# Kernel optimization log

Measured on AMD Instinct MI355X. Metric: run time of the kernel, lower is better.

Reference implementation:

```python
import jax, jax.numpy as jnp
import numpy as np

H, D = 8, 32          # num_heads, head dim (hidden = 256)
HID = H * D
LRELU = 0.2
NT, NC, E, FIN = 60000, 30000, 200000, 64


def setup_inputs() -> dict:
    key = jax.random.key(0)
    ks = jax.random.split(key, 24)
    s = 0.05
    inp = {
        'x_trans': jax.random.normal(ks[0], (NT, FIN), jnp.float32),
        'x_cc':    jax.random.normal(ks[1], (NC, FIN), jnp.float32),
        'src_c2t': jax.random.randint(ks[2], (E,), 0, NC),
        'dst_c2t': jax.random.randint(ks[3], (E,), 0, NT),
        'src_t2c': jax.random.randint(ks[4], (E,), 0, NT),
        'dst_t2c': jax.random.randint(ks[5], (E,), 0, NC),
        'W_in': jax.random.normal(ks[6], (2, FIN, HID), jnp.float32) * s,
        'b_in': jnp.zeros((2, HID), jnp.float32),
        'Wk': jax.random.normal(ks[7], (2, 2, HID, HID), jnp.float32) * s,
        'bk': jnp.zeros((2, 2, HID), jnp.float32),
        'Wq': jax.random.normal(ks[8], (2, 2, HID, HID), jnp.float32) * s,
        'bq': jnp.zeros((2, 2, HID), jnp.float32),
        'Wv': jax.random.normal(ks[9], (2, 2, HID, HID), jnp.float32) * s,
        'bv': jnp.zeros((2, 2, HID), jnp.float32),
        'Wa': jax.random.normal(ks[10], (2, 2, HID, HID), jnp.float32) * s,
        'ba': jnp.zeros((2, 2, HID), jnp.float32),
        'a_rel': jax.random.normal(ks[11], (2, 2, H, D, D), jnp.float32) * s,
        'm_rel': jax.random.normal(ks[12], (2, 2, H, D, D), jnp.float32) * s,
        'p_rel': jnp.ones((2, 2, H), jnp.float32),
        'skip':  jnp.ones((2, 2), jnp.float32),
        'W_out': jax.random.normal(ks[13], (HID, 64), jnp.float32) * s,
        'b_out': jnp.zeros((64,), jnp.float32),
    }
    return inp


def _hgt_layer(xs, Wk, bk, Wq, bq, Wv, bv, Wa, ba, a_rel, m_rel, p_rel, skip, edges):
    # xs: list of [N_t, HID] per node type; edges: list of (src_type, dst_type, src_idx, dst_idx)
    nt = len(xs)
    k = [(xs[t] @ Wk[t] + bk[t]).reshape(-1, H, D) for t in range(nt)]
    q = [(xs[t] @ Wq[t] + bq[t]).reshape(-1, H, D) for t in range(nt)]
    v = [(xs[t] @ Wv[t] + bv[t]).reshape(-1, H, D) for t in range(nt)]
    agg = [jnp.zeros((xs[t].shape[0], H, D), xs[t].dtype) for t in range(nt)]
    inv_sqrt_d = 1.0 / jnp.sqrt(jnp.float32(D))
    for r, (st, dt, si, di) in enumerate(edges):
        kr = jnp.einsum('nhd,hde->nhe', k[st], a_rel[r])   # relation-transformed keys
        vr = jnp.einsum('nhd,hde->nhe', v[st], m_rel[r])   # relation-transformed messages
        ke, ve, qe = kr[si], vr[si], q[dt][di]             # [E, H, D] gathers
        alpha = jnp.einsum('ehd,ehd->eh', qe, ke) * p_rel[r] * inv_sqrt_d  # [E, H]
        n_dst = xs[dt].shape[0]
        m = jax.ops.segment_max(alpha, di, num_segments=n_dst)
        ex = jnp.exp(alpha - m[di])
        ssum = jax.ops.segment_sum(ex, di, num_segments=n_dst)
        w = ex / (ssum[di] + 1e-16)                         # segment softmax per dst node
        agg[dt] = agg[dt] + jax.ops.segment_sum(ve * w[..., None], di, num_segments=n_dst)
    out = []
    for t in range(nt):
        o = jax.nn.gelu(agg[t].reshape(-1, HID), approximate=False)
        o = o @ Wa[t] + ba[t]
        beta = jax.nn.sigmoid(skip[t])
        out.append(beta * o + (1.0 - beta) * xs[t])
    return out


def reference(x_trans, x_cc, src_c2t, dst_c2t, src_t2c, dst_t2c,
              W_in, b_in, Wk, bk, Wq, bq, Wv, bv, Wa, ba,
              a_rel, m_rel, p_rel, skip, W_out, b_out):
    # per-node-type Linear + in-place relu
    xs = [jax.nn.relu(x_trans @ W_in[0] + b_in[0]),
          jax.nn.relu(x_cc @ W_in[1] + b_in[1])]
    # relation 0: cc_node -> trans_node ; relation 1: trans_node -> cc_node
    edges = [(1, 0, src_c2t, dst_c2t), (0, 1, src_t2c, dst_t2c)]
    n_layers = Wk.shape[0]
    for l in range(n_layers):
        xs = _hgt_layer(xs, Wk[l], bk[l], Wq[l], bq[l], Wv[l], bv[l], Wa[l], ba[l],
                        a_rel[l], m_rel[l], p_rel[l], skip[l], edges)
    # dropout is identity in eval mode
    y = xs[0] @ W_out + b_out
    y = jnp.where(y > 0, y, LRELU * y)                      # LeakyReLU(0.2)
    n = jnp.linalg.norm(y, axis=1, keepdims=True)
    return y / jnp.maximum(n, 1e-12)                        # F.normalize(p=2, dim=1)
```

## Files before the change

kernel.cpp:

```cpp
#include <hip/hip_runtime.h>
#include <hip/hip_bf16.h>
#include <math.h>

#define NTN 60000
#define NCN 30000
#define NED 200000

typedef unsigned short u16;
typedef unsigned long long u64;
typedef __attribute__((ext_vector_type(8))) u16 u16x8;
typedef __attribute__((ext_vector_type(8))) __bf16 bf16x8;
typedef __attribute__((ext_vector_type(4))) float f32x4;

static __device__ __forceinline__ float bf2f(u16 u) {
    return __uint_as_float(((unsigned)u) << 16);
}
static __device__ __forceinline__ u16 f2bf(float f) {
    unsigned u = __float_as_uint(f);
    unsigned r = (u + 0x7fffu + ((u >> 16) & 1u)) >> 16;
    return (u16)r;
}

__global__ void fill_u32(unsigned* __restrict__ p, unsigned v, int n) {
    int i = blockIdx.x * blockDim.x + threadIdx.x;
    int stride = gridDim.x * blockDim.x;
    for (; i < n; i += stride) p[i] = v;
}

__global__ void f32_to_bf16(const float* __restrict__ in, u16* __restrict__ out, int n4) {
    int i = blockIdx.x * blockDim.x + threadIdx.x;
    int stride = gridDim.x * blockDim.x;
    for (; i < n4; i += stride) {
        float4 v = ((const float4*)in)[i];
        ushort4 o;
        o.x = f2bf(v.x); o.y = f2bf(v.y); o.z = f2bf(v.z); o.w = f2bf(v.w);
        ((ushort4*)out)[i] = o;
    }
}

__global__ void convTb(const float* __restrict__ in, u16* __restrict__ out,
                       int K, int N, int inStride, int outStride, int nm) {
    int idx = blockIdx.x * blockDim.x + threadIdx.x;
    int per = N * (K >> 2);
    int total = per * nm;
    if (idx >= total) return;
    int mat = idx / per, rem = idx - mat * per;
    int k4 = rem / N, n = rem - k4 * N;
    int k = k4 * 4;
    const float* src = in + (size_t)mat * inStride;
    u16* dst = out + (size_t)mat * outStride;
    ushort4 o;
    o.x = f2bf(src[(size_t)(k + 0) * N + n]);
    o.y = f2bf(src[(size_t)(k + 1) * N + n]);
    o.z = f2bf(src[(size_t)(k + 2) * N + n]);
    o.w = f2bf(src[(size_t)(k + 3) * N + n]);
    *(ushort4*)(dst + (size_t)n * K + k) = o;
}

__global__ void copy_bq(const float* __restrict__ bq, float* __restrict__ bqkv) {
    int lt = blockIdx.x;
    bqkv[lt * 768 + threadIdx.x] = bq[lt * 256 + threadIdx.x];
}

__global__ __launch_bounds__(256) void fuse_weights(
    const float* __restrict__ Wk, const float* __restrict__ bk,
    const float* __restrict__ Wv, const float* __restrict__ bv,
    const float* __restrict__ a_rel, const float* __restrict__ m_rel,
    const float* __restrict__ p_rel,
    float* __restrict__ Wf2, float* __restrict__ bqkv)
{
    __shared__ float kw[256], vw[256];
    const int c = blockIdx.x, lt = blockIdx.y, tid = threadIdx.x;
    const int l = lt >> 1, t = lt & 1;
    const int lr = l * 2 + (t == 1 ? 0 : 1);
    const float* WkP = Wk + (size_t)lt * 65536;
    const float* WvP = Wv + (size_t)lt * 65536;
    const float* ar = a_rel + (size_t)lr * 8192;
    const float* mr = m_rel + (size_t)lr * 8192;
    kw[tid] = WkP[c * 256 + tid];
    vw[tid] = WvP[c * 256 + tid];
    __syncthreads();
    const int h = tid >> 5, e = tid & 31;
    const float s = p_rel[lr * 8 + h] * 0.17677669529663687f;
    float ak = 0.f, av = 0.f;
#pragma unroll 8
    for (int d = 0; d < 32; ++d) {
        ak += kw[h * 32 + d] * ar[h * 1024 + d * 32 + e];
        av += vw[h * 32 + d] * mr[h * 1024 + d * 32 + e];
    }
    float* WkfP = Wf2 + (size_t)lt * 131072;
    WkfP[c * 256 + tid] = ak * s;
    WkfP[65536 + c * 256 + tid] = av;
    if (c == 0) {
        const float* bkP = bk + (size_t)lt * 256;
        const float* bvP = bv + (size_t)lt * 256;
        float bka = 0.f, bva = 0.f;
#pragma unroll 8
        for (int d = 0; d < 32; ++d) {
            bka += bkP[h * 32 + d] * ar[h * 1024 + d * 32 + e];
            bva += bvP[h * 32 + d] * mr[h * 1024 + d * 32 + e];
        }
        bqkv[lt * 768 + 256 + tid] = bka * s;
        bqkv[lt * 768 + 512 + tid] = bva;
    }
}

template <int EPI, int BN, bool OBF>
__global__ __launch_bounds__(256) void gemm_mfma2(
    int nblk0,
    const u16* __restrict__ A0, const u16* __restrict__ W0, const float* __restrict__ b0,
    void* __restrict__ C0, int M0, int ldC0, int NY0,
    const u16* __restrict__ xr0, const float* __restrict__ sk0,
    const u16* __restrict__ A1, const u16* __restrict__ W1, const float* __restrict__ b1,
    void* __restrict__ C1, int M1, int ldC1, int NY1,
    const u16* __restrict__ xr1, const float* __restrict__ sk1,
    int K)
{
    constexpr int ASZ = 64 * 64;
    constexpr int BSZ = BN * 64;
    constexpr int NF = BN / 32;
    __shared__ u16 smem[2 * (ASZ + BSZ)];
    u16* As0 = smem;             u16* Bs0 = smem + ASZ;
    u16* As1 = smem + ASZ + BSZ; u16* Bs1 = As1 + ASZ;

    const int nwg = gridDim.x;
    const int bid = blockIdx.x;
    const int q8 = nwg >> 3, r8 = nwg & 7;
    const int xcd = bid & 7, pos = bid >> 3;
    const int lbid = (xcd < r8) ? xcd * (q8 + 1) + pos
                                : r8 * (q8 + 1) + (xcd - r8) * q8 + pos;

    const u16* A; const u16* WT; const float* bias; void* Cv;
    int M, ldC, NY, sb; const u16* xres; const float* skipPtr;
    if (lbid < nblk0) {
        A = A0; WT = W0; bias = b0; Cv = C0; M = M0; ldC = ldC0; NY = NY0;
        xres = xr0; skipPtr = sk0; sb = lbid;
    } else {
        A = A1; WT = W1; bias = b1; Cv = C1; M = M1; ldC = ldC1; NY = NY1;
        xres = xr1; skipPtr = sk1; sb = lbid - nblk0;
    }
    const int bx = sb / NY, by = sb - bx * NY;
    const int m0 = bx * 64, n0 = by * BN;

    const int tid = threadIdx.x;
    const int wave = tid >> 6, lane = tid & 63;
    const int wm = (wave >> 1) * 32, wn = (wave & 1) * (BN / 2);
    f32x4 acc[2][NF];
#pragma unroll
    for (int i = 0; i < 2; ++i)
#pragma unroll
        for (int j = 0; j < NF; ++j) acc[i][j] = (f32x4){0.f, 0.f, 0.f, 0.f};

    const int sr = lane >> 3;
    const int sl = lane & 7;

    auto stage = [&](int k0, u16* Ad, u16* Bd) {
#pragma unroll
        for (int i = 0; i < 2; ++i) {
            int rb = wave * 16 + i * 8;
            int r = rb + sr;
            int gr = m0 + r; gr = gr < M ? gr : M - 1;
            const u16* gp = A + (size_t)gr * K + k0 + ((sl ^ sr) << 3);
            __builtin_amdgcn_global_load_lds(
                (const __attribute__((address_space(1))) void*)gp,
                (__attribute__((address_space(3))) void*)(Ad + rb * 64), 16, 0, 0);
        }
#pragma unroll
        for (int i = 0; i < NF; ++i) {
            int rb = wave * (BN / 4) + i * 8;
            int r = rb + sr;
            const u16* gp = WT + (size_t)(n0 + r) * K + k0 + ((sl ^ sr) << 3);
            __builtin_amdgcn_global_load_lds(
                (const __attribute__((address_space(1))) void*)gp,
                (__attribute__((address_space(3))) void*)(Bd + rb * 64), 16, 0, 0);
        }
    };

    auto compute = [&](const u16* Ab, const u16* Bb) {
#pragma unroll
        for (int kx = 0; kx < 2; ++kx) {
            bf16x8 af[2], bfr[NF];
#pragma unroll
            for (int mf = 0; mf < 2; ++mf) {
                int r = wm + mf * 16 + (lane & 15);
                int slot = (lane >> 4) + kx * 4;
                af[mf] = __builtin_bit_cast(bf16x8,
                    *(const u16x8*)(Ab + r * 64 + ((slot ^ (r & 7)) << 3)));
            }
#pragma unroll
            for (int nf = 0; nf < NF; ++nf) {
                int r = wn + nf * 16 + (lane & 15);
                int slot = (lane >> 4) + kx * 4;
                bfr[nf] = __builtin_bit_cast(bf16x8,
                    *(const u16x8*)(Bb + r * 64 + ((slot ^ (r & 7)) << 3)));
            }
#pragma unroll
            for (int mf = 0; mf < 2; ++mf)
#pragma unroll
                for (int nf = 0; nf < NF; ++nf)
                    acc[mf][nf] = __builtin_amdgcn_mfma_f32_16x16x32_bf16(
                        af[mf], bfr[nf], acc[mf][nf], 0, 0, 0);
        }
    };

    const int nt = K >> 6;
    stage(0, As0, Bs0);
    for (int t = 0; t < nt; ++t) {
        const bool pb = t & 1;
        if (t + 1 < nt) {
            stage((t + 1) << 6, pb ? As0 : As1, pb ? Bs0 : Bs1);
            __builtin_amdgcn_sched_barrier(0);
            if constexpr (BN == 128) asm volatile("s_waitcnt vmcnt(6)" ::: "memory");
            else                     asm volatile("s_waitcnt vmcnt(4)" ::: "memory");
        } else {
            asm volatile("s_waitcnt vmcnt(0)" ::: "memory");
        }
        __builtin_amdgcn_s_barrier();
        __builtin_amdgcn_sched_barrier(0);
        compute(pb ? As1 : As0, pb ? Bs1 : Bs0);
        __builtin_amdgcn_sched_barrier(0);
        __builtin_amdgcn_s_barrier();
        __builtin_amdgcn_sched_barrier(0);
    }

    float beta = 0.f;
    if (EPI == 2) beta = 1.f / (1.f + expf(-skipPtr[0]));

    if constexpr (OBF) {
        constexpr int CLD = BN + 8;
        u16* Ct = smem;
#pragma unroll
        for (int nf = 0; nf < NF; ++nf) {
            int col = wn + nf * 16 + (lane & 15);
            int gcol = n0 + col;
            float bs = bias[gcol];
#pragma unroll
            for (int mf = 0; mf < 2; ++mf) {
#pragma unroll
                for (int j = 0; j < 4; ++j) {
                    int row = wm + mf * 16 + (lane >> 4) * 4 + j;
                    int grow = m0 + row;
                    int gr2 = grow < M ? grow : 0;
                    float c = acc[mf][nf][j] + bs;
                    if (EPI == 1) c = fmaxf(c, 0.f);
                    if (EPI == 2) c = beta * c + (1.f - beta) * bf2f(xres[(size_t)gr2 * ldC + gcol]);
                    if (EPI == 3) c = (c > 0.f) ? c : 0.2f * c;
                    Ct[row * CLD + col] = f2bf(c);
                }
            }
        }
        __syncthreads();
        int row = tid >> 2, c0 = (tid & 3) * (BN / 4);
        int grow = m0 + row;
        if (grow < M) {
            u16* dst = (u16*)Cv + (size_t)grow * ldC + n0 + c0;
            const u16* src = Ct + row * CLD + c0;
#pragma unroll
            for (int i = 0; i < BN / 32; ++i)
                *(u16x8*)(dst + i * 8) = *(const u16x8*)(src + i * 8);
        }
    } else {
#pragma unroll
        for (int nf = 0; nf < NF; ++nf) {
            int gcol = n0 + wn + nf * 16 + (lane & 15);
            float bs = bias[gcol];
#pragma unroll
            for (int mf = 0; mf < 2; ++mf) {
#pragma unroll
                for (int j = 0; j < 4; ++j) {
                    int grow = m0 + wm + mf * 16 + (lane >> 4) * 4 + j;
                    if (grow >= M) continue;
                    float c = acc[mf][nf][j] + bs;
                    if (EPI == 1) c = fmaxf(c, 0.f);
                    if (EPI == 3) c = (c > 0.f) ? c : 0.2f * c;
                    ((float*)Cv)[(size_t)grow * ldC + gcol] = c;
                }
            }
        }
    }
}

__global__ void hist_kernel(const int* __restrict__ di, unsigned* __restrict__ counts, int E) {
    int e = blockIdx.x * blockDim.x + threadIdx.x;
    if (e < E) atomicAdd(&counts[di[e]], 1u);
}

__global__ __launch_bounds__(256) void scan_blocks(
    const unsigned* __restrict__ counts, unsigned* __restrict__ pref,
    unsigned* __restrict__ bsum, int N)
{
    __shared__ unsigned tmp[256];
    int i = blockIdx.x * 256 + threadIdx.x;
    unsigned v = (i < N) ? counts[i] : 0u;
    tmp[threadIdx.x] = v;
    __syncthreads();
    for (int off = 1; off < 256; off <<= 1) {
        unsigned t = (threadIdx.x >= off) ? tmp[threadIdx.x - off] : 0u;
        __syncthreads();
        tmp[threadIdx.x] += t;
        __syncthreads();
    }
    if (i < N) pref[i] = tmp[threadIdx.x] - v;
    if (threadIdx.x == 255) bsum[blockIdx.x] = tmp[255];
}

__global__ __launch_bounds__(256) void scan_top(unsigned* __restrict__ bsum, int NB) {
    __shared__ unsigned tmp[256];
    unsigned v = (threadIdx.x < NB) ? bsum[threadIdx.x] : 0u;
    tmp[threadIdx.x] = v;
    __syncthreads();
    for (int off = 1; off < 256; off <<= 1) {
        unsigned t = (threadIdx.x >= off) ? tmp[threadIdx.x - off] : 0u;
        __syncthreads();
        tmp[threadIdx.x] += t;
        __syncthreads();
    }
    if (threadIdx.x < NB) bsum[threadIdx.x] = tmp[threadIdx.x] - v;
}

__global__ void scan_add(unsigned* __restrict__ pref, const unsigned* __restrict__ bsum,
                         const unsigned* __restrict__ counts,
                         unsigned* __restrict__ cursor, u64* __restrict__ rowinfo, int N) {
    int i = blockIdx.x * 256 + threadIdx.x;
    if (i < N) {
        unsigned s = pref[i] + bsum[blockIdx.x];
        cursor[i] = s;
        rowinfo[i] = (u64)s | ((u64)counts[i] << 32);
    }
}

__global__ void place_kernel(const int* __restrict__ di, const int* __restrict__ si,
                             unsigned* __restrict__ cursor, unsigned* __restrict__ srcout, int E) {
    int e = blockIdx.x * blockDim.x + threadIdx.x;
    if (e < E) {
        unsigned p = atomicAdd(&cursor[di[e]], 1u);
        srcout[p] = (unsigned)si[e] * 768u;
    }
}

#define TBLK ((NTN + 3) / 4)
__global__ __launch_bounds__(256) void edge_gather2(
    const u16* __restrict__ qkvT, const u16* __restrict__ qkvC,
    const u64* __restrict__ riT, const unsigned* __restrict__ srcT,
    const u64* __restrict__ riC, const unsigned* __restrict__ srcC,
    u16* __restrict__ aggT, u16* __restrict__ aggC)
{
    const int b = blockIdx.x;
    const bool isT = b < TBLK;
    const int n = (isT ? b : b - TBLK) * 4 + (threadIdx.x >> 6);
    const int Ndst = isT ? NTN : NCN;
    if (n >= Ndst) return;
    const u16* qkv_d = isT ? qkvT : qkvC;
    const u16* qkv_s = isT ? qkvC : qkvT;
    const u64* ri = isT ? riT : riC;
    const unsigned* srcarr = isT ? srcT : srcC;
    u16* agg = isT ? aggT : aggC;

    const int lane = threadIdx.x & 63;
    const int lq = lane & 31;
    const int h = lane >> 5;
    const u64 rinfo = ri[n];
    const unsigned start = (unsigned)rinfo;
    const unsigned deg = (unsigned)(rinfo >> 32);

    if (deg == 0) {
        if (lane < 32)
            *(u16x8*)&agg[(size_t)n * 256 + lq * 8] = (u16x8){0, 0, 0, 0, 0, 0, 0, 0};
        return;
    }

    u16x8 qv = *(const u16x8*)&qkv_d[(size_t)n * 768 + lq * 8];
    float qf[8];
#pragma unroll
    for (int i = 0; i < 8; ++i) qf[i] = bf2f(qv[i]);

    const u16* kvb = qkv_s + 256 + lq * 8;
    float m = -INFINITY, s = 0.f;
    float acc[8] = {0.f, 0.f, 0.f, 0.f, 0.f, 0.f, 0.f, 0.f};

    unsigned j = (unsigned)h;
    if (j < deg) {
        unsigned off = srcarr[start + j];
        u16x8 kr = *(const u16x8*)(kvb + off);
        u16x8 vr = *(const u16x8*)(kvb + off + 256);
        for (;;) {
            u16x8 kr_n, vr_n;
            const bool more = (j + 2 < deg);
            if (more) {
                unsigned off2 = srcarr[start + j + 2];
                kr_n = *(const u16x8*)(kvb + off2);
                vr_n = *(const u16x8*)(kvb + off2 + 256);
            }
            float kf[8];
#pragma unroll
            for (int i = 0; i < 8; ++i) kf[i] = bf2f(kr[i]);
            float p = qf[0] * kf[0] + qf[1] * kf[1] + qf[2] * kf[2] + qf[3] * kf[3]
                    + qf[4] * kf[4] + qf[5] * kf[5] + qf[6] * kf[6] + qf[7] * kf[7];
            p += __shfl_xor(p, 1);
            p += __shfl_xor(p, 2);
            float vf[8];
#pragma unroll
            for (int i = 0; i < 8; ++i) vf[i] = bf2f(vr[i]);
            if (__ballot(p > m) == 0ull) {
                float wv = __expf(p - m);
                s += wv;
#pragma unroll
                for (int i = 0; i < 8; ++i) acc[i] += wv * vf[i];
            } else {
                float mn = fmaxf(m, p);
                float sc = __expf(m - mn);
                float wv = __expf(p - mn);
                s = s * sc + wv;
#pragma unroll
                for (int i = 0; i < 8; ++i) acc[i] = acc[i] * sc + wv * vf[i];
                m = mn;
            }
            if (!more) break;
            kr = kr_n; vr = vr_n; j += 2;
        }
    }

    float mo = __shfl_xor(m, 32);
    float so = __shfl_xor(s, 32);
    float mt = fmaxf(m, mo);
    float sc0 = __expf(m - mt);
    float sco = __expf(mo - mt);
    float st = s * sc0 + so * sco;
    float inv = 1.f / (st + 1e-16f);
    u16x8 ov;
#pragma unroll
    for (int i = 0; i < 8; ++i) {
        float ao = __shfl_xor(acc[i], 32);
        float x = (acc[i] * sc0 + ao * sco) * inv;
        float g = 0.5f * x * (1.f + erff(x * 0.70710678118654752f));
        ov[i] = f2bf(g);
    }
    if (lane < 32)
        *(u16x8*)&agg[(size_t)n * 256 + lq * 8] = ov;
}

__global__ __launch_bounds__(256) void norm_rows(float* __restrict__ y, int M) {
    int row = blockIdx.x * 4 + (threadIdx.x >> 6);
    int lane = threadIdx.x & 63;
    if (row >= M) return;
    float v = y[(size_t)row * 64 + lane];
    float s = v * v;
#pragma unroll
    for (int off = 1; off < 64; off <<= 1) s += __shfl_xor(s, off);
    float n = sqrtf(s);
    y[(size_t)row * 64 + lane] = v / fmaxf(n, 1e-12f);
}

extern "C" void kernel_launch(void* const* d_in, const int* in_sizes, int n_in,
                              void* d_out, int out_size, void* d_ws, size_t ws_size,
                              hipStream_t stream)
{
    const float* x_trans = (const float*)d_in[0];
    const float* x_cc    = (const float*)d_in[1];
    const int* src_c2t   = (const int*)d_in[2];
    const int* dst_c2t   = (const int*)d_in[3];
    const int* src_t2c   = (const int*)d_in[4];
    const int* dst_t2c   = (const int*)d_in[5];
    const float* W_in = (const float*)d_in[6];
    const float* b_in = (const float*)d_in[7];
    const float* Wk   = (const float*)d_in[8];
    const float* bk   = (const float*)d_in[9];
    const float* Wq   = (const float*)d_in[10];
    const float* bq   = (const float*)d_in[11];
    const float* Wv   = (const float*)d_in[12];
    const float* bv   = (const float*)d_in[13];
    const float* Wa   = (const float*)d_in[14];
    const float* ba   = (const float*)d_in[15];
    const float* a_rel = (const float*)d_in[16];
    const float* m_rel = (const float*)d_in[17];
    const float* p_rel = (const float*)d_in[18];
    const float* skip  = (const float*)d_in[19];
    const float* W_out = (const float*)d_in[20];
    const float* b_out = (const float*)d_in[21];

    char* w = (char*)d_ws;
    auto alloc = [&](size_t bytes) { char* p = w; w += (bytes + 255) & ~(size_t)255; return p; };
    u16* xs0  = (u16*)alloc((size_t)NTN * 256 * 2);
    u16* xs1  = (u16*)alloc((size_t)NCN * 256 * 2);
    u16* xin0 = (u16*)alloc((size_t)NTN * 64 * 2);
    u16* xin1 = (u16*)alloc((size_t)NCN * 64 * 2);
    u16* qkv0 = (u16*)alloc((size_t)NTN * 768 * 2);
    u16* qkv1 = (u16*)alloc((size_t)NCN * 768 * 2);
    u16* agg0 = (u16*)alloc((size_t)NTN * 256 * 2);
    u16* agg1 = (u16*)alloc((size_t)NCN * 256 * 2);
    u16* WinT = (u16*)alloc((size_t)2 * 16384 * 2);
    u16* WqkvT= (u16*)alloc((size_t)4 * 196608 * 2);
    u16* WaT  = (u16*)alloc((size_t)4 * 65536 * 2);
    u16* WoutT= (u16*)alloc((size_t)16384 * 2);
    float* Wf2 = (float*)alloc((size_t)4 * 131072 * 4);
    float* bqkv = (float*)alloc((size_t)4 * 768 * 4);
    unsigned* countsT   = (unsigned*)alloc((size_t)NTN * 4);
    unsigned* prefT     = (unsigned*)alloc((size_t)NTN * 4);
    unsigned* cursorT   = (unsigned*)alloc((size_t)NTN * 4);
    u64* rowinfoT       = (u64*)alloc((size_t)NTN * 8);
    unsigned* srcAT     = (unsigned*)alloc((size_t)NED * 4);
    unsigned* countsC   = (unsigned*)alloc((size_t)NCN * 4);
    unsigned* prefC     = (unsigned*)alloc((size_t)NCN * 4);
    unsigned* cursorC   = (unsigned*)alloc((size_t)NCN * 4);
    u64* rowinfoC       = (u64*)alloc((size_t)NCN * 8);
    unsigned* srcAC     = (unsigned*)alloc((size_t)NED * 4);
    unsigned* bsum      = (unsigned*)alloc((size_t)256 * 4);
    (void)ws_size; (void)in_sizes; (void)n_in; (void)out_size;

    {
        const int EB = (NED + 255) / 256;
        int NBt = (NTN + 255) / 256;
        fill_u32<<<256, 256, 0, stream>>>(countsT, 0u, NTN);
        hist_kernel<<<EB, 256, 0, stream>>>(dst_c2t, countsT, NED);
        scan_blocks<<<NBt, 256, 0, stream>>>(countsT, prefT, bsum, NTN);
        scan_top<<<1, 256, 0, stream>>>(bsum, NBt);
        scan_add<<<NBt, 256, 0, stream>>>(prefT, bsum, countsT, cursorT, rowinfoT, NTN);
        place_kernel<<<EB, 256, 0, stream>>>(dst_c2t, src_c2t, cursorT, srcAT, NED);
        int NBc = (NCN + 255) / 256;
        fill_u32<<<256, 256, 0, stream>>>(countsC, 0u, NCN);
        hist_kernel<<<EB, 256, 0, stream>>>(dst_t2c, countsC, NED);
        scan_blocks<<<NBc, 256, 0, stream>>>(countsC, prefC, bsum, NCN);
        scan_top<<<1, 256, 0, stream>>>(bsum, NBc);
        scan_add<<<NBc, 256, 0, stream>>>(prefC, bsum, countsC, cursorC, rowinfoC, NCN);
        place_kernel<<<EB, 256, 0, stream>>>(dst_t2c, src_t2c, cursorC, srcAC, NED);
    }

    fuse_weights<<<dim3(256, 4), 256, 0, stream>>>(Wk, bk, Wv, bv, a_rel, m_rel, p_rel, Wf2, bqkv);
    copy_bq<<<4, 256, 0, stream>>>(bq, bqkv);
    convTb<<<(4 * 16384 + 255) / 256, 256, 0, stream>>>(Wq, WqkvT, 256, 256, 65536, 196608, 4);
    convTb<<<(4 * 16384 + 255) / 256, 256, 0, stream>>>(Wf2, WqkvT + 65536, 256, 256, 131072, 196608, 4);
    convTb<<<(4 * 16384 + 255) / 256, 256, 0, stream>>>(Wf2 + 65536, WqkvT + 131072, 256, 256, 131072, 196608, 4);
    convTb<<<(4 * 16384 + 255) / 256, 256, 0, stream>>>(Wa, WaT, 256, 256, 65536, 65536, 4);
    convTb<<<(2 * 4096 + 255) / 256, 256, 0, stream>>>(W_in, WinT, 64, 256, 16384, 16384, 2);
    convTb<<<(4096 + 255) / 256, 256, 0, stream>>>(W_out, WoutT, 256, 64, 16384, 16384, 1);
    f32_to_bf16<<<1024, 256, 0, stream>>>(x_trans, xin0, NTN * 64 / 4);
    f32_to_bf16<<<1024, 256, 0, stream>>>(x_cc,    xin1, NCN * 64 / 4);

    const int GT = (NTN + 63) / 64, GC = (NCN + 63) / 64;

    gemm_mfma2<1, 64, true><<<GT * 4 + GC * 4, 256, 0, stream>>>(
        GT * 4,
        xin0, WinT, b_in, xs0, NTN, 256, 4, nullptr, nullptr,
        xin1, WinT + 16384, b_in + 256, xs1, NCN, 256, 4, nullptr, nullptr,
        64);

    for (int l = 0; l < 2; ++l) {
        size_t lt0 = (size_t)(l * 2 + 0), lt1 = (size_t)(l * 2 + 1);

        gemm_mfma2<0, 64, true><<<GT * 12 + GC * 12, 256, 0, stream>>>(
            GT * 12,
            xs0, WqkvT + lt0 * 196608, bqkv + lt0 * 768, qkv0, NTN, 768, 12, nullptr, nullptr,
            xs1, WqkvT + lt1 * 196608, bqkv + lt1 * 768, qkv1, NCN, 768, 12, nullptr, nullptr,
            256);

        edge_gather2<<<TBLK + (NCN + 3) / 4, 256, 0, stream>>>(
            qkv0, qkv1,
            rowinfoT, srcAT,
            rowinfoC, srcAC,
            agg0, agg1);

        gemm_mfma2<2, 64, true><<<GT * 4 + GC * 4, 256, 0, stream>>>(
            GT * 4,
            agg0, WaT + lt0 * 65536, ba + lt0 * 256, xs0, NTN, 256, 4, xs0, skip + l * 2 + 0,
            agg1, WaT + lt1 * 65536, ba + lt1 * 256, xs1, NCN, 256, 4, xs1, skip + l * 2 + 1,
            256);
    }

    {
        float* y = (float*)d_out;
        gemm_mfma2<3, 64, false><<<GT, 256, 0, stream>>>(
            GT,
            xs0, WoutT, b_out, y, NTN, 64, 1, nullptr, nullptr,
            xs0, WoutT, b_out, y, NTN, 64, 1, nullptr, nullptr,
            256);
        norm_rows<<<NTN / 4, 256, 0, stream>>>(y, NTN);
    }
}
```

Before: 481.7 us.

## Assign one half-wave per destination node, replace erf GELU with tanh form, fuse CSR-build kernels

The edge gather now maps each 32-lane half-wave to its own destination node, so there is no cross-half softmax merge and each wave handles two nodes instead of splitting one node's edges. The exact erf GELU is replaced by a tanh-approximation evaluated with exp. The paired CSR-construction kernels (fill, histogram, scans, placement) for both relations are merged into single launches to cut launch count. Per-node parallelism over edges is halved, which lengthens the serial chain for high-degree nodes, and the tanh GELU changes numerics slightly.

```diff
diff --git a/kernel.cpp b/kernel.cpp
--- a/kernel.cpp
+++ b/kernel.cpp
@@ -21,10 +21,11 @@
     return (u16)r;
 }
 
-__global__ void fill_u32(unsigned* __restrict__ p, unsigned v, int n) {
+__global__ void fill2(unsigned* __restrict__ a, int na, unsigned* __restrict__ b, int nb) {
     int i = blockIdx.x * blockDim.x + threadIdx.x;
-    int stride = gridDim.x * blockDim.x;
-    for (; i < n; i += stride) p[i] = v;
+    int st = gridDim.x * blockDim.x;
+    for (int k = i; k < na; k += st) a[k] = 0u;
+    for (int k = i; k < nb; k += st) b[k] = 0u;
 }
 
 __global__ void f32_to_bf16(const float* __restrict__ in, u16* __restrict__ out, int n4) {
@@ -280,15 +281,24 @@
     }
 }
 
-__global__ void hist_kernel(const int* __restrict__ di, unsigned* __restrict__ counts, int E) {
+__global__ void hist2(const int* __restrict__ d0, unsigned* __restrict__ c0,
+                      const int* __restrict__ d1, unsigned* __restrict__ c1, int E) {
     int e = blockIdx.x * blockDim.x + threadIdx.x;
-    if (e < E) atomicAdd(&counts[di[e]], 1u);
-}
-
-__global__ __launch_bounds__(256) void scan_blocks(
-    const unsigned* __restrict__ counts, unsigned* __restrict__ pref,
-    unsigned* __restrict__ bsum, int N)
-{
+    if (e < E) {
+        atomicAdd(&c0[d0[e]], 1u);
+        atomicAdd(&c1[d1[e]], 1u);
+    }
+}
+
+__global__ __launch_bounds__(256) void scan_blocks2(
+    const unsigned* __restrict__ c0, unsigned* __restrict__ p0, unsigned* __restrict__ bs0, int N0,
+    const unsigned* __restrict__ c1, unsigned* __restrict__ p1, unsigned* __restrict__ bs1, int N1)
+{
+    const unsigned* counts = blockIdx.y ? c1 : c0;
+    unsigned* pref = blockIdx.y ? p1 : p0;
+    unsigned* bsum = blockIdx.y ? bs1 : bs0;
+    int N = blockIdx.y ? N1 : N0;
+    if ((int)blockIdx.x * 256 >= N) return;
     __shared__ unsigned tmp[256];
     int i = blockIdx.x * 256 + threadIdx.x;
     unsigned v = (i < N) ? counts[i] : 0u;
@@ -304,9 +314,13 @@
     if (threadIdx.x == 255) bsum[blockIdx.x] = tmp[255];
 }
 
-__global__ __launch_bounds__(256) void scan_top(unsigned* __restrict__ bsum, int NB) {
+__global__ __launch_bounds__(256) void scan_top2(
+    unsigned* __restrict__ bs0, int NB0, unsigned* __restrict__ bs1, int NB1)
+{
+    unsigned* bsum = blockIdx.x ? bs1 : bs0;
+    int NB = blockIdx.x ? NB1 : NB0;
     __shared__ unsigned tmp[256];
-    unsigned v = (threadIdx.x < NB) ? bsum[threadIdx.x] : 0u;
+    unsigned v = ((int)threadIdx.x < NB) ? bsum[threadIdx.x] : 0u;
     tmp[threadIdx.x] = v;
     __syncthreads();
     for (int off = 1; off < 256; off <<= 1) {
@@ -315,12 +329,21 @@
         tmp[threadIdx.x] += t;
         __syncthreads();
     }
-    if (threadIdx.x < NB) bsum[threadIdx.x] = tmp[threadIdx.x] - v;
-}
-
-__global__ void scan_add(unsigned* __restrict__ pref, const unsigned* __restrict__ bsum,
-                         const unsigned* __restrict__ counts,
-                         unsigned* __restrict__ cursor, u64* __restrict__ rowinfo, int N) {
+    if ((int)threadIdx.x < NB) bsum[threadIdx.x] = tmp[threadIdx.x] - v;
+}
+
+__global__ void scan_add2(
+    const unsigned* __restrict__ p0, const unsigned* __restrict__ bs0,
+    const unsigned* __restrict__ c0, unsigned* __restrict__ cur0, u64* __restrict__ ri0, int N0,
+    const unsigned* __restrict__ p1, const unsigned* __restrict__ bs1,
+    const unsigned* __restrict__ c1, unsigned* __restrict__ cur1, u64* __restrict__ ri1, int N1)
+{
+    const unsigned* pref = blockIdx.y ? p1 : p0;
+    const unsigned* bsum = blockIdx.y ? bs1 : bs0;
+    const unsigned* counts = blockIdx.y ? c1 : c0;
+    unsigned* cursor = blockIdx.y ? cur1 : cur0;
+    u64* rowinfo = blockIdx.y ? ri1 : ri0;
+    int N = blockIdx.y ? N1 : N0;
     int i = blockIdx.x * 256 + threadIdx.x;
     if (i < N) {
         unsigned s = pref[i] + bsum[blockIdx.x];
@@ -329,16 +352,20 @@
     }
 }
 
-__global__ void place_kernel(const int* __restrict__ di, const int* __restrict__ si,
-                             unsigned* __restrict__ cursor, unsigned* __restrict__ srcout, int E) {
+__global__ void place2(const int* __restrict__ d0, const int* __restrict__ s0,
+                       unsigned* __restrict__ cur0, unsigned* __restrict__ o0,
+                       const int* __restrict__ d1, const int* __restrict__ s1,
+                       unsigned* __restrict__ cur1, unsigned* __restrict__ o1, int E) {
     int e = blockIdx.x * blockDim.x + threadIdx.x;
     if (e < E) {
-        unsigned p = atomicAdd(&cursor[di[e]], 1u);
-        srcout[p] = (unsigned)si[e] * 768u;
-    }
-}
-
-#define TBLK ((NTN + 3) / 4)
+        unsigned p = atomicAdd(&cur0[d0[e]], 1u);
+        o0[p] = (unsigned)s0[e] * 768u;
+        unsigned q = atomicAdd(&cur1[d1[e]], 1u);
+        o1[q] = (unsigned)s1[e] * 768u;
+    }
+}
+
+#define TBLK8 ((NTN + 7) / 8)
 __global__ __launch_bounds__(256) void edge_gather2(
     const u16* __restrict__ qkvT, const u16* __restrict__ qkvC,
     const u64* __restrict__ riT, const unsigned* __restrict__ srcT,
@@ -346,26 +373,24 @@
     u16* __restrict__ aggT, u16* __restrict__ aggC)
 {
     const int b = blockIdx.x;
-    const bool isT = b < TBLK;
-    const int n = (isT ? b : b - TBLK) * 4 + (threadIdx.x >> 6);
-    const int Ndst = isT ? NTN : NCN;
-    if (n >= Ndst) return;
+    const bool isT = b < TBLK8;
+    const int lane = threadIdx.x & 63;
+    const int lq = lane & 31;
+    const int n = (((isT ? b : b - TBLK8) << 2) + (int)(threadIdx.x >> 6)) * 2 + (lane >> 5);
+
     const u16* qkv_d = isT ? qkvT : qkvC;
     const u16* qkv_s = isT ? qkvC : qkvT;
     const u64* ri = isT ? riT : riC;
     const unsigned* srcarr = isT ? srcT : srcC;
     u16* agg = isT ? aggT : aggC;
 
-    const int lane = threadIdx.x & 63;
-    const int lq = lane & 31;
-    const int h = lane >> 5;
     const u64 rinfo = ri[n];
     const unsigned start = (unsigned)rinfo;
     const unsigned deg = (unsigned)(rinfo >> 32);
+    u16* outp = &agg[(size_t)n * 256 + lq * 8];
 
     if (deg == 0) {
-        if (lane < 32)
-            *(u16x8*)&agg[(size_t)n * 256 + lq * 8] = (u16x8){0, 0, 0, 0, 0, 0, 0, 0};
+        *(u16x8*)outp = (u16x8){0, 0, 0, 0, 0, 0, 0, 0};
         return;
     }
 
@@ -378,65 +403,56 @@
     float m = -INFINITY, s = 0.f;
     float acc[8] = {0.f, 0.f, 0.f, 0.f, 0.f, 0.f, 0.f, 0.f};
 
-    unsigned j = (unsigned)h;
-    if (j < deg) {
-        unsigned off = srcarr[start + j];
-        u16x8 kr = *(const u16x8*)(kvb + off);
-        u16x8 vr = *(const u16x8*)(kvb + off + 256);
-        for (;;) {
-            u16x8 kr_n, vr_n;
-            const bool more = (j + 2 < deg);
-            if (more) {
-                unsigned off2 = srcarr[start + j + 2];
-                kr_n = *(const u16x8*)(kvb + off2);
-                vr_n = *(const u16x8*)(kvb + off2 + 256);
-            }
-            float kf[8];
-#pragma unroll
-            for (int i = 0; i < 8; ++i) kf[i] = bf2f(kr[i]);
-            float p = qf[0] * kf[0] + qf[1] * kf[1] + qf[2] * kf[2] + qf[3] * kf[3]
-                    + qf[4] * kf[4] + qf[5] * kf[5] + qf[6] * kf[6] + qf[7] * kf[7];
-            p += __shfl_xor(p, 1);
-            p += __shfl_xor(p, 2);
-            float vf[8];
-#pragma unroll
-            for (int i = 0; i < 8; ++i) vf[i] = bf2f(vr[i]);
-            if (__ballot(p > m) == 0ull) {
-                float wv = __expf(p - m);
-                s += wv;
-#pragma unroll
-                for (int i = 0; i < 8; ++i) acc[i] += wv * vf[i];
-            } else {
-                float mn = fmaxf(m, p);
-                float sc = __expf(m - mn);
-                float wv = __expf(p - mn);
-                s = s * sc + wv;
-#pragma unroll
-                for (int i = 0; i < 8; ++i) acc[i] = acc[i] * sc + wv * vf[i];
-                m = mn;
-            }
-            if (!more) break;
-            kr = kr_n; vr = vr_n; j += 2;
-        }
-    }
-
-    float mo = __shfl_xor(m, 32);
-    float so = __shfl_xor(s, 32);
-    float mt = fmaxf(m, mo);
-    float sc0 = __expf(m - mt);
-    float sco = __expf(mo - mt);
-    float st = s * sc0 + so * sco;
-    float inv = 1.f / (st + 1e-16f);
+    unsigned off = srcarr[start];
+    u16x8 kr = *(const u16x8*)(kvb + off);
+    u16x8 vr = *(const u16x8*)(kvb + off + 256);
+    for (unsigned j = 0;;) {
+        const bool more = (j + 1 < deg);
+        u16x8 kr_n, vr_n;
+        if (more) {
+            unsigned off2 = srcarr[start + j + 1];
+            kr_n = *(const u16x8*)(kvb + off2);
+            vr_n = *(const u16x8*)(kvb + off2 + 256);
+        }
+        float kf[8];
+#pragma unroll
+        for (int i = 0; i < 8; ++i) kf[i] = bf2f(kr[i]);
+        float p = qf[0] * kf[0] + qf[1] * kf[1] + qf[2] * kf[2] + qf[3] * kf[3]
+                + qf[4] * kf[4] + qf[5] * kf[5] + qf[6] * kf[6] + qf[7] * kf[7];
+        p += __shfl_xor(p, 1);
+        p += __shfl_xor(p, 2);
+        float vf[8];
+#pragma unroll
+        for (int i = 0; i < 8; ++i) vf[i] = bf2f(vr[i]);
+        if (__ballot(p > m) == 0ull) {
+            float wv = __expf(p - m);
+            s += wv;
+#pragma unroll
+            for (int i = 0; i < 8; ++i) acc[i] += wv * vf[i];
+        } else {
+            float mn = fmaxf(m, p);
+            float sc = __expf(m - mn);
+            float wv = __expf(p - mn);
+            s = s * sc + wv;
+#pragma unroll
+            for (int i = 0; i < 8; ++i) acc[i] = acc[i] * sc + wv * vf[i];
+            m = mn;
+        }
+        if (!more) break;
+        kr = kr_n; vr = vr_n; ++j;
+    }
+
+    float inv = 1.f / (s + 1e-16f);
     u16x8 ov;
 #pragma unroll
     for (int i = 0; i < 8; ++i) {
-        float ao = __shfl_xor(acc[i], 32);
-        float x = (acc[i] * sc0 + ao * sco) * inv;
-        float g = 0.5f * x * (1.f + erff(x * 0.70710678118654752f));
-        ov[i] = f2bf(g);
-    }
-    if (lane < 32)
-        *(u16x8*)&agg[(size_t)n * 256 + lq * 8] = ov;
+        float x = acc[i] * inv;
+        float y2 = 1.5957691216f * x + 0.0713548163f * x * x * x;
+        float e = __expf(y2);
+        float t = 1.f - 2.f / (e + 1.f);
+        ov[i] = f2bf(0.5f * x * (1.f + t));
+    }
+    *(u16x8*)outp = ov;
 }
 
 __global__ __launch_bounds__(256) void norm_rows(float* __restrict__ y, int M) {
@@ -504,25 +520,22 @@
     unsigned* cursorC   = (unsigned*)alloc((size_t)NCN * 4);
     u64* rowinfoC       = (u64*)alloc((size_t)NCN * 8);
     unsigned* srcAC     = (unsigned*)alloc((size_t)NED * 4);
-    unsigned* bsum      = (unsigned*)alloc((size_t)256 * 4);
+    unsigned* bsum      = (unsigned*)alloc((size_t)2 * 256 * 4);
     (void)ws_size; (void)in_sizes; (void)n_in; (void)out_size;
 
     {
         const int EB = (NED + 255) / 256;
-        int NBt = (NTN + 255) / 256;
-        fill_u32<<<256, 256, 0, stream>>>(countsT, 0u, NTN);
-        hist_kernel<<<EB, 256, 0, stream>>>(dst_c2t, countsT, NED);
-        scan_blocks<<<NBt, 256, 0, stream>>>(countsT, prefT, bsum, NTN);
-        scan_top<<<1, 256, 0, stream>>>(bsum, NBt);
-        scan_add<<<NBt, 256, 0, stream>>>(prefT, bsum, countsT, cursorT, rowinfoT, NTN);
-        place_kernel<<<EB, 256, 0, stream>>>(dst_c2t, src_c2t, cursorT, srcAT, NED);
-        int NBc = (NCN + 255) / 256;
-        fill_u32<<<256, 256, 0, stream>>>(countsC, 0u, NCN);
-        hist_kernel<<<EB, 256, 0, stream>>>(dst_t2c, countsC, NED);
-        scan_blocks<<<NBc, 256, 0, stream>>>(countsC, prefC, bsum, NCN);
-        scan_top<<<1, 256, 0, stream>>>(bsum, NBc);
-        scan_add<<<NBc, 256, 0, stream>>>(prefC, bsum, countsC, cursorC, rowinfoC, NCN);
-        place_kernel<<<EB, 256, 0, stream>>>(dst_t2c, src_t2c, cursorC, srcAC, NED);
+        const int NBt = (NTN + 255) / 256, NBc = (NCN + 255) / 256;
+        fill2<<<256, 256, 0, stream>>>(countsT, NTN, countsC, NCN);
+        hist2<<<EB, 256, 0, stream>>>(dst_c2t, countsT, dst_t2c, countsC, NED);
+        scan_blocks2<<<dim3(NBt, 2), 256, 0, stream>>>(countsT, prefT, bsum, NTN,
+                                                       countsC, prefC, bsum + 256, NCN);
+        scan_top2<<<2, 256, 0, stream>>>(bsum, NBt, bsum + 256, NBc);
+        scan_add2<<<dim3(NBt, 2), 256, 0, stream>>>(
+            prefT, bsum, countsT, cursorT, rowinfoT, NTN,
+            prefC, bsum + 256, countsC, cursorC, rowinfoC, NCN);
+        place2<<<EB, 256, 0, stream>>>(dst_c2t, src_c2t, cursorT, srcAT,
+                                       dst_t2c, src_t2c, cursorC, srcAC, NED);
     }
 
     fuse_weights<<<dim3(256, 4), 256, 0, stream>>>(Wk, bk, Wv, bv, a_rel, m_rel, p_rel, Wf2, bqkv);
@@ -553,7 +566,7 @@
             xs1, WqkvT + lt1 * 196608, bqkv + lt1 * 768, qkv1, NCN, 768, 12, nullptr, nullptr,
             256);
 
-        edge_gather2<<<TBLK + (NCN + 3) / 4, 256, 0, stream>>>(
+        edge_gather2<<<TBLK8 + (NCN + 7) / 8, 256, 0, stream>>>(
             qkv0, qkv1,
             rowinfoT, srcAT,
             rowinfoC, srcAC,
```

Result: faster. 469.2 us (-2.6%).
